# Kernel tuning notes

Measured on AMD Instinct MI355X. Metric: run time of the kernel, lower is better.

Reference implementation:

```python
import jax, jax.numpy as jnp
import numpy as np

B, L, C = 4, 2048, 1024

def setup_inputs() -> dict:
    key = jax.random.key(0)
    k1, k2, k3 = jax.random.split(key, 3)
    net_in = jax.random.normal(k1, (B, L, C), dtype=jnp.float32)
    # torch Linear weights stored as (out, in); we keep that convention
    w_qkv = jax.random.normal(k2, (3 * C, C), dtype=jnp.float32) * (1.0 / np.sqrt(C))
    w_out = jax.random.normal(k3, (C, C), dtype=jnp.float32) * (1.0 / np.sqrt(C))
    return {"net_in": net_in, "w_qkv": w_qkv, "w_out": w_out}

def reference(net_in, w_qkv, w_out):
    Bc, Lc, Cc = net_in.shape
    qkv = jnp.einsum('blc,dc->bld', net_in, w_qkv)  # (B, L, 3C)
    q, k, v = jnp.split(qkv, 3, axis=-1)
    attn = jnp.einsum('bqc,bkc->bqk', q, k) / jnp.sqrt(jnp.float32(Cc))
    causal = jnp.tril(jnp.ones((Lc, Lc), dtype=bool))
    attn = jnp.where(causal[None, :, :], attn, -jnp.inf)
    attn = jax.nn.softmax(attn, axis=-1)
    out = jnp.einsum('bqk,bkc->bqc', attn, v)
    return jnp.einsum('blc,dc->bld', out, w_out)
```

## Files before the change

### kernel.cpp

```cpp
#include <hip/hip_runtime.h>
#include <hip/hip_bf16.h>
#include <cstdint>
#include <cstddef>

typedef __hip_bfloat16 bf16;
typedef float  floatx4 __attribute__((ext_vector_type(4)));
typedef __bf16 bf16x8  __attribute__((ext_vector_type(8)));

typedef __attribute__((address_space(1))) void as1_void;
typedef __attribute__((address_space(3))) void as3_void;

constexpr int Bn = 4, Ln = 2048, Cn = 1024;

__device__ __forceinline__ void store_one(float* p, float v) { *p = v; }
__device__ __forceinline__ void store_one(bf16*  p, float v) { *p = __float2bfloat16(v); }

#define BAR()    asm volatile("s_barrier" ::: "memory")
#define VMCNT2() asm volatile("s_waitcnt vmcnt(2)" ::: "memory")
#define VMCNT0() asm volatile("s_waitcnt vmcnt(0)" ::: "memory")
#define SCHEDB() __builtin_amdgcn_sched_barrier(0)
#define STAGE(gp, off) \
    __builtin_amdgcn_global_load_lds((const as1_void*)(gp), (as3_void*)(smem + (off)), 16, 0, 0)

__device__ __forceinline__ void gemm256_core(
    char* __restrict__ smem,
    const bf16* __restrict__ A, const bf16* __restrict__ B,
    int m0, int n0, int kbeg, int kend, int lda, int ldb,
    floatx4 (&acc)[8][4])
{
    const int tid  = threadIdx.x;
    const int lane = tid & 63;
    const int quad = lane >> 4;
    const int lr   = lane & 15;
    const int wave = tid >> 6;
    const int wm   = (wave >> 2) * 128;
    const int wn   = (wave & 3) * 64;

#pragma unroll
    for (int i = 0; i < 8; ++i)
#pragma unroll
        for (int j = 0; j < 4; ++j) { floatx4 z = {0.f, 0.f, 0.f, 0.f}; acc[i][j] = z; }

    const int srow = tid >> 3;
    const int sx   = (tid & 7) ^ (srow & 7);
    const bf16* gA = A + (size_t)(m0 + srow) * lda + sx * 8 + kbeg;
    const bf16* gB = B + (size_t)(n0 + srow) * ldb + sx * 8 + kbeg;
    const int wuni = __builtin_amdgcn_readfirstlane((tid & 0x1C0) * 16);

    const int aoff = (wm + lr) * 64;
    const int boff = (wn + lr) * 64;
    const int s0   = (quad ^ (lr & 7)) * 8;

    const int NT = (kend - kbeg) >> 6;

    STAGE(gB,             32768 + 0 * 8192 + wuni);
    STAGE(gB + 64  * ldb, 32768 + 1 * 8192 + wuni);
    STAGE(gB + 128 * ldb, 32768 + 2 * 8192 + wuni);
    STAGE(gB + 192 * ldb, 32768 + 3 * 8192 + wuni);
    STAGE(gA,                     0 * 8192 + wuni);
    STAGE(gA + 128 * lda,         2 * 8192 + wuni);
    STAGE(gA + 64  * lda,         1 * 8192 + wuni);
    STAGE(gA + 192 * lda,         3 * 8192 + wuni);
    VMCNT2();
    BAR();

#define LDA4(MB, SK) do { _Pragma("unroll") for (int ii = 0; ii < 4; ++ii) \
        a[ii] = *(const bf16x8*)(As + aoff + ((MB) * 4 + ii) * 1024 + (SK)); } while (0)
#define LDB4(SK) do { _Pragma("unroll") for (int nn = 0; nn < 4; ++nn) \
        b[nn] = *(const bf16x8*)(Bs + boff + nn * 1024 + (SK)); } while (0)
#define MFMA16(MB) do { _Pragma("unroll") for (int ii = 0; ii < 4; ++ii) { \
        _Pragma("unroll") for (int nn = 0; nn < 4; ++nn) \
            acc[(MB) * 4 + ii][nn] = __builtin_amdgcn_mfma_f32_16x16x32_bf16( \
                a[ii], b[nn], acc[(MB) * 4 + ii][nn], 0, 0, 0); } } while (0)

    for (int t = 0; t < NT; ++t) {
        const bf16* As = (const bf16*)(smem + (t & 1) * 65536);
        const bf16* Bs = (const bf16*)(smem + (t & 1) * 65536 + 32768);
        const int  wl  = ((t + 1) & 1) * 65536;
        const int  kn  = (t + 1) << 6;
        const bool more = (t + 1 < NT);
        bf16x8 a[4], b[4];

        LDB4(s0);
        LDA4(0, s0);
        if (more) {
            STAGE(gB + kn,            wl + 32768 + 0 * 8192 + wuni);
            STAGE(gB + kn + 64 * ldb, wl + 32768 + 1 * 8192 + wuni);
        }
        BAR(); SCHEDB();
        __builtin_amdgcn_s_setprio(1);
        MFMA16(0);
        __builtin_amdgcn_s_setprio(0);
        SCHEDB();
        if (more) VMCNT2(); else VMCNT0();
        BAR();

        LDA4(1, s0);
        if (more) {
            STAGE(gB + kn + 128 * ldb, wl + 32768 + 2 * 8192 + wuni);
            STAGE(gB + kn + 192 * ldb, wl + 32768 + 3 * 8192 + wuni);
        }
        BAR(); SCHEDB();
        __builtin_amdgcn_s_setprio(1);
        MFMA16(1);
        __builtin_amdgcn_s_setprio(0);
        SCHEDB();
        BAR();

        LDB4(s0 ^ 32);
        LDA4(0, s0 ^ 32);
        if (more) {
            STAGE(gA + kn,             wl + 0 * 8192 + wuni);
            STAGE(gA + kn + 128 * lda, wl + 2 * 8192 + wuni);
        }
        BAR(); SCHEDB();
        __builtin_amdgcn_s_setprio(1);
        MFMA16(0);
        __builtin_amdgcn_s_setprio(0);
        SCHEDB();
        BAR();

        LDA4(1, s0 ^ 32);
        if (more) {
            STAGE(gA + kn + 64  * lda, wl + 1 * 8192 + wuni);
            STAGE(gA + kn + 192 * lda, wl + 3 * 8192 + wuni);
        }
        BAR(); SCHEDB();
        __builtin_amdgcn_s_setprio(1);
        MFMA16(1);
        __builtin_amdgcn_s_setprio(0);
        SCHEDB();
        if (more) VMCNT2();
        BAR();
    }
#undef LDA4
#undef LDB4
#undef MFMA16
}

template <typename OutT>
__device__ __forceinline__ void gemm256(
    char* __restrict__ smem,
    const bf16* __restrict__ A, const bf16* __restrict__ B, OutT* __restrict__ C,
    int m0, int n0, int kbeg, int kend, int lda, int ldb, int ldc, float cscale)
{
    floatx4 acc[8][4];
    gemm256_core(smem, A, B, m0, n0, kbeg, kend, lda, ldb, acc);

    const int lane = threadIdx.x & 63;
    const int quad = lane >> 4;
    const int lr   = lane & 15;
    const int wave = threadIdx.x >> 6;
    const int wm   = (wave >> 2) * 128;
    const int wn   = (wave & 3) * 64;

#pragma unroll
    for (int mi = 0; mi < 8; ++mi) {
        const int row = m0 + wm + mi * 16 + quad * 4;
#pragma unroll
        for (int n = 0; n < 4; ++n) {
            const int col = n0 + wn + n * 16 + lr;
            OutT* cp = C + (size_t)row * ldc + col;
#pragma unroll
            for (int r = 0; r < 4; ++r)
                store_one(cp + (size_t)r * ldc, acc[mi][n][r] * cscale);
        }
    }
}

__global__ __launch_bounds__(512, 2)
void g1_qk(const bf16* __restrict__ Xb, const bf16* __restrict__ Wqkb,
           bf16* __restrict__ QK)
{
    __shared__ __align__(16) char smem[131072];
    const int i = blockIdx.x;
    const int j = i >> 3;
    const int mt = (i & 7) * 4 + (j & 3);
    const int nt = j >> 2;
    gemm256<bf16>(smem, Xb, Wqkb, QK, mt * 256, nt * 256, 0, 1024, 1024, 1024, 2048, 1.0f);
}

__global__ __launch_bounds__(512, 2)
void g2_s_w2(const bf16* __restrict__ QK, const bf16* __restrict__ Wob,
             const bf16* __restrict__ WvT, bf16* __restrict__ S,
             bf16* __restrict__ W2)
{
    __shared__ __align__(16) char smem[131072];
    const int i = blockIdx.x;
    if (i < 144) {
        const int b = (i & 7) >> 1;
        const int t = (i >> 3) * 2 + (i & 1);
        int ti = (int)((sqrtf(8.f * t + 1.f) - 1.f) * 0.5f);
        while ((ti + 1) * (ti + 2) / 2 <= t) ++ti;
        while (ti * (ti + 1) / 2 > t) --ti;
        const int tj = t - ti * (ti + 1) / 2;
        const bf16* Aq = QK + (size_t)b * Ln * 2048;
        const bf16* Bk = Aq + 1024;
        bf16* Sb = S + (size_t)b * Ln * Ln;
        gemm256<bf16>(smem, Aq, Bk, Sb, ti * 256, tj * 256, 0, 1024, 2048, 2048, Ln, 0.03125f);
    } else {
        const int j = i - 144;
        gemm256<bf16>(smem, Wob, WvT, W2, (j & 3) * 256, (j >> 2) * 256, 0, 1024, 1024, 1024, 1024, 1.0f);
    }
}

__device__ __forceinline__ float waveMax(float x) {
#pragma unroll
    for (int o = 32; o > 0; o >>= 1) x = fmaxf(x, __shfl_xor(x, o, 64));
    return x;
}
__device__ __forceinline__ float waveSum(float x) {
#pragma unroll
    for (int o = 32; o > 0; o >>= 1) x += __shfl_xor(x, o, 64);
    return x;
}

__device__ void softmax_rows(bf16* __restrict__ S, int row0)
{
    const int wave = threadIdx.x >> 6, lane = threadIdx.x & 63;
    for (int it8 = 0; it8 < 8; ++it8) {
        const int row = row0 + wave * 8 + it8;
        const int q = row & (Ln - 1);
        bf16* Srow = S + (size_t)row * Ln;
        const int kmax = ((q >> 7) + 1) << 7;
        const int nv = (kmax + 511) >> 9;
        float x[4][8];
        float m = -1e30f;
        for (int it = 0; it < nv; ++it) {
            int c0 = it * 512 + lane * 8;
            bf16x8 v = *(const bf16x8*)(Srow + c0);
#pragma unroll
            for (int e = 0; e < 8; ++e) {
                float f = (float)v[e];
                f = (c0 + e <= q) ? f : -1e30f;
                x[it][e] = f;
                m = fmaxf(m, f);
            }
        }
        m = waveMax(m);
        float s = 0.f;
        for (int it = 0; it < nv; ++it)
#pragma unroll
            for (int e = 0; e < 8; ++e) {
                float ex = (x[it][e] > -1e29f) ? __expf(x[it][e] - m) : 0.f;
                x[it][e] = ex;
                s += ex;
            }
        s = waveSum(s);
        const float inv = 1.f / s;
        for (int it = 0; it < nv; ++it) {
            bf16x8 o;
#pragma unroll
            for (int e = 0; e < 8; ++e) o[e] = (__bf16)(x[it][e] * inv);
            *(bf16x8*)(Srow + it * 512 + lane * 8) = o;
        }
    }
}

__global__ __launch_bounds__(512, 2)
void g3_vwt_sm(const bf16* __restrict__ W2, const bf16* __restrict__ Xb,
               bf16* __restrict__ VWT, bf16* __restrict__ S)
{
    __shared__ __align__(16) char smem[131072];
    const int i = blockIdx.x;
    if (i < 128) {
        const int j = i >> 3;
        const int nt = (i & 7) * 4 + (j & 3);
        const int mt = j >> 2;
        gemm256<bf16>(smem, W2, Xb, VWT, mt * 256, nt * 256, 0, 1024, 1024, 1024, 8192, 1.0f);
    } else {
        softmax_rows(S, (i - 128) * 64);
    }
}

__global__ __launch_bounds__(512, 2)
void g4_out(const bf16* __restrict__ P, const bf16* __restrict__ VWT,
            float* __restrict__ out)
{
    __shared__ __align__(16) char smem[131072];
    const int i = blockIdx.x;
    const int r = i & 7;
    const int b = r >> 1, p = r & 1;
    const int q = i >> 3;
    const int nt = p * 2 + (q & 1);
    const int j = q >> 1;

    const bf16* Pp = P + (size_t)b * Ln * Ln;
    const bf16* Bv = VWT + (size_t)b * Ln;
    float* Co = out + (size_t)b * Ln * Cn;
    const int n0 = nt * 256;

    if (j < 4) {
        gemm256<float>(smem, Pp, Bv, Co, j * 256, n0, 0, (j + 1) * 256, Ln, 8192, Cn, 1.0f);
        return;
    }

    const int mt   = 4 + ((j - 4) >> 1);
    const int c    = (j - 4) & 1;
    const int half = ((mt + 1) * 256) >> 1;
    const int kb   = c * half;
    const int m0   = mt * 256;

    floatx4 acc[8][4];
    gemm256_core(smem, Pp, Bv, m0, n0, kb, kb + half, Ln, 8192, acc);

    const int lane = threadIdx.x & 63;
    const int quad = lane >> 4;
    const int lr   = lane & 15;
    const int wave = threadIdx.x >> 6;
    const int wm   = (wave >> 2) * 128;
    const int wn   = (wave & 3) * 64;

#pragma unroll
    for (int mi = 0; mi < 8; ++mi) {
        const int row = m0 + wm + mi * 16 + quad * 4;
#pragma unroll
        for (int n = 0; n < 4; ++n) {
            const int col = n0 + wn + n * 16 + lr;
            float* cp = Co + (size_t)row * Cn + col;
#pragma unroll
            for (int rr = 0; rr < 4; ++rr)
                unsafeAtomicAdd(cp + (size_t)rr * Cn, acc[mi][n][rr]);
        }
    }
}

__global__ __launch_bounds__(256)
void cast_all(const float* __restrict__ X, const float* __restrict__ Wqkv,
              const float* __restrict__ Wo,
              bf16* __restrict__ Xb, bf16* __restrict__ Wqkb,
              bf16* __restrict__ Wob, bf16* __restrict__ WvT,
              float* __restrict__ out)
{
    int blk = blockIdx.x;
    if (blk < 11264) {
        int i = blk * 256 + threadIdx.x;
        const float* src; bf16* dst; int off;
        if (i < 2097152)                 { src = X;    dst = Xb;   off = i; }
        else if (i < 2097152 + 524288)   { src = Wqkv; dst = Wqkb; off = i - 2097152; }
        else                             { src = Wo;   dst = Wob;  off = i - 2621440; }
        float4 f = ((const float4*)src)[off];
        bf16 o0 = __float2bfloat16(f.x), o1 = __float2bfloat16(f.y);
        bf16 o2 = __float2bfloat16(f.z), o3 = __float2bfloat16(f.w);
        ushort4 u;
        u.x = *(unsigned short*)&o0; u.y = *(unsigned short*)&o1;
        u.z = *(unsigned short*)&o2; u.w = *(unsigned short*)&o3;
        *(ushort4*)(dst + (size_t)off * 4) = u;
    } else if (blk < 12288) {
        __shared__ float t[32][33];
        int tt = blk - 11264;
        int c0 = (tt & 31) * 32;
        int r0 = (tt >> 5) * 32;
        const float* Wv = Wqkv + 2048 * 1024;
        int xcol = threadIdx.x & 31, y0 = threadIdx.x >> 5;
#pragma unroll
        for (int p = 0; p < 4; ++p) {
            int y = y0 + 8 * p;
            t[y][xcol] = Wv[(size_t)(r0 + y) * 1024 + c0 + xcol];
        }
        __syncthreads();
#pragma unroll
        for (int p = 0; p < 4; ++p) {
            int mloc = y0 + 8 * p;
            WvT[(size_t)(c0 + mloc) * 1024 + r0 + xcol] = __float2bfloat16(t[xcol][mloc]);
        }
    } else {
        int t = (blk - 12288) * 256 + threadIdx.x;
        float4* o4 = (float4*)out;
        float4 z = {0.f, 0.f, 0.f, 0.f};
#pragma unroll
        for (int p = 0; p < 4; ++p)
            o4[(size_t)p * 524288 + 262144 + t] = z;
    }
}

extern "C" void kernel_launch(void* const* d_in, const int* in_sizes, int n_in,
                              void* d_out, int out_size, void* d_ws, size_t ws_size,
                              hipStream_t stream)
{
    const float* X    = (const float*)d_in[0];
    const float* Wqkv = (const float*)d_in[1];
    const float* Wout = (const float*)d_in[2];
    float* out = (float*)d_out;

    char* ws = (char*)d_ws;
    const size_t MiB = 1024ull * 1024ull;
    bf16* Xb   = (bf16*)(ws + 0);
    bf16* QK   = (bf16*)(ws + 16 * MiB);
    bf16* VWT  = (bf16*)(ws + 48 * MiB);
    bf16* Sbuf = (bf16*)(ws + 64 * MiB);
    bf16* Wqkb = (bf16*)(ws + 96 * MiB);
    bf16* WvT  = (bf16*)(ws + 100 * MiB);
    bf16* Wob  = (bf16*)(ws + 102 * MiB);
    bf16* W2   = (bf16*)(ws + 104 * MiB);

    cast_all<<<dim3(13312), 256, 0, stream>>>(X, Wqkv, Wout, Xb, Wqkb, Wob, WvT, out);

    g1_qk<<<dim3(256), 512, 0, stream>>>(Xb, Wqkb, QK);

    g2_s_w2<<<dim3(160), 512, 0, stream>>>(QK, Wob, WvT, Sbuf, W2);

    g3_vwt_sm<<<dim3(256), 512, 0, stream>>>(W2, Xb, VWT, Sbuf);

    g4_out<<<dim3(192), 512, 0, stream>>>(Sbuf, VWT, out);
}
```

Before: 239.4 us.

## Replace split-K atomic PV GEMM with 256x128 tiles and direct stores

The final P·VWT GEMM now uses a new 256x128-tile kernel over 256 blocks, each covering the full causal K range for its row tile. This replaces 256x256 tiles where the later row tiles were split in K and summed with float atomics. Because every output is now written exactly once, the zero-fill of the output in the cast kernel is removed. The trade-off is more total A-tile loads (each P row tile is read by twice as many column tiles) and uneven work across blocks, since late row tiles run long K loops without splitting. LDS use drops to 96KB.

```diff
diff --git a/kernel.cpp b/kernel.cpp
--- a/kernel.cpp
+++ b/kernel.cpp
@@ -164,6 +164,130 @@
 #pragma unroll
             for (int r = 0; r < 4; ++r)
                 store_one(cp + (size_t)r * ldc, acc[mi][n][r] * cscale);
+        }
+    }
+}
+
+__device__ __forceinline__ void gemm_pv_128n(
+    char* __restrict__ smem,
+    const bf16* __restrict__ A, const bf16* __restrict__ B, float* __restrict__ C,
+    int m0, int n0, int kend, int lda, int ldb, int ldc)
+{
+    const int tid  = threadIdx.x;
+    const int lane = tid & 63;
+    const int quad = lane >> 4;
+    const int lr   = lane & 15;
+    const int wave = tid >> 6;
+    const int wm   = (wave >> 2) * 128;
+    const int wn   = (wave & 3) * 32;
+
+    floatx4 acc[8][2];
+#pragma unroll
+    for (int i = 0; i < 8; ++i)
+#pragma unroll
+        for (int j = 0; j < 2; ++j) { floatx4 z = {0.f, 0.f, 0.f, 0.f}; acc[i][j] = z; }
+
+    const int srow = tid >> 3;
+    const int sx   = (tid & 7) ^ (srow & 7);
+    const bf16* gA = A + (size_t)(m0 + srow) * lda + sx * 8;
+    const bf16* gB = B + (size_t)(n0 + srow) * ldb + sx * 8;
+    const int wuni = __builtin_amdgcn_readfirstlane((tid & 0x1C0) * 16);
+
+    const int aoff = (wm + lr) * 64;
+    const int boff = (wn + lr) * 64;
+    const int s0   = (quad ^ (lr & 7)) * 8;
+
+    const int NT = kend >> 6;
+    const int BUF = 49152;
+
+    STAGE(gB,             32768 + 0 * 8192 + wuni);
+    STAGE(gB + 64  * ldb, 32768 + 1 * 8192 + wuni);
+    STAGE(gA,                     0 * 8192 + wuni);
+    STAGE(gA + 128 * lda,         2 * 8192 + wuni);
+    STAGE(gA + 64  * lda,         1 * 8192 + wuni);
+    STAGE(gA + 192 * lda,         3 * 8192 + wuni);
+    VMCNT2();
+    BAR();
+
+#define LDA4(MB, SK) do { _Pragma("unroll") for (int ii = 0; ii < 4; ++ii) \
+        a[ii] = *(const bf16x8*)(As + aoff + ((MB) * 4 + ii) * 1024 + (SK)); } while (0)
+#define LDB2(SK) do { _Pragma("unroll") for (int nn = 0; nn < 2; ++nn) \
+        b[nn] = *(const bf16x8*)(Bs + boff + nn * 1024 + (SK)); } while (0)
+#define MFMA8(MB) do { _Pragma("unroll") for (int ii = 0; ii < 4; ++ii) { \
+        _Pragma("unroll") for (int nn = 0; nn < 2; ++nn) \
+            acc[(MB) * 4 + ii][nn] = __builtin_amdgcn_mfma_f32_16x16x32_bf16( \
+                a[ii], b[nn], acc[(MB) * 4 + ii][nn], 0, 0, 0); } } while (0)
+
+    for (int t = 0; t < NT; ++t) {
+        const bf16* As = (const bf16*)(smem + (t & 1) * BUF);
+        const bf16* Bs = (const bf16*)(smem + (t & 1) * BUF + 32768);
+        const int  wl  = ((t + 1) & 1) * BUF;
+        const int  kn  = (t + 1) << 6;
+        const bool more = (t + 1 < NT);
+        bf16x8 a[4], b[2];
+
+        LDB2(s0);
+        LDA4(0, s0);
+        if (more) {
+            STAGE(gB + kn,            wl + 32768 + 0 * 8192 + wuni);
+            STAGE(gB + kn + 64 * ldb, wl + 32768 + 1 * 8192 + wuni);
+        }
+        BAR(); SCHEDB();
+        __builtin_amdgcn_s_setprio(1);
+        MFMA8(0);
+        __builtin_amdgcn_s_setprio(0);
+        SCHEDB();
+        if (more) VMCNT2(); else VMCNT0();
+        BAR();
+
+        LDA4(1, s0);
+        if (more) {
+            STAGE(gA + kn,             wl + 0 * 8192 + wuni);
+            STAGE(gA + kn + 128 * lda, wl + 2 * 8192 + wuni);
+        }
+        BAR(); SCHEDB();
+        __builtin_amdgcn_s_setprio(1);
+        MFMA8(1);
+        __builtin_amdgcn_s_setprio(0);
+        SCHEDB();
+        BAR();
+
+        LDB2(s0 ^ 32);
+        LDA4(0, s0 ^ 32);
+        if (more) {
+            STAGE(gA + kn + 64  * lda, wl + 1 * 8192 + wuni);
+            STAGE(gA + kn + 192 * lda, wl + 3 * 8192 + wuni);
+        }
+        BAR(); SCHEDB();
+        __builtin_amdgcn_s_setprio(1);
+        MFMA8(0);
+        __builtin_amdgcn_s_setprio(0);
+        SCHEDB();
+        BAR();
+
+        LDA4(1, s0 ^ 32);
+        BAR(); SCHEDB();
+        __builtin_amdgcn_s_setprio(1);
+        MFMA8(1);
+        __builtin_amdgcn_s_setprio(0);
+        SCHEDB();
+        if (more) VMCNT2();
+        BAR();
+    }
+#undef LDA4
+#undef LDB2
+#undef MFMA8
+
+#pragma unroll
+    for (int mi = 0; mi < 8; ++mi) {
+        const int row = m0 + wm + mi * 16 + quad * 4;
+#pragma unroll
+        for (int n = 0; n < 2; ++n) {
+            const int col = n0 + wn + n * 16 + lr;
+            float* cp = C + (size_t)row * ldc + col;
+#pragma unroll
+            for (int r = 0; r < 4; ++r)
+                cp[(size_t)r * ldc] = acc[mi][n][r];
         }
     }
 }
@@ -277,60 +401,25 @@
 void g4_out(const bf16* __restrict__ P, const bf16* __restrict__ VWT,
             float* __restrict__ out)
 {
-    __shared__ __align__(16) char smem[131072];
+    __shared__ __align__(16) char smem[98304];
     const int i = blockIdx.x;
     const int r = i & 7;
     const int b = r >> 1, p = r & 1;
     const int q = i >> 3;
-    const int nt = p * 2 + (q & 1);
-    const int j = q >> 1;
+    const int nt = p * 4 + (q & 3);
+    const int mt = q >> 2;
 
     const bf16* Pp = P + (size_t)b * Ln * Ln;
     const bf16* Bv = VWT + (size_t)b * Ln;
     float* Co = out + (size_t)b * Ln * Cn;
-    const int n0 = nt * 256;
-
-    if (j < 4) {
-        gemm256<float>(smem, Pp, Bv, Co, j * 256, n0, 0, (j + 1) * 256, Ln, 8192, Cn, 1.0f);
-        return;
-    }
-
-    const int mt   = 4 + ((j - 4) >> 1);
-    const int c    = (j - 4) & 1;
-    const int half = ((mt + 1) * 256) >> 1;
-    const int kb   = c * half;
-    const int m0   = mt * 256;
-
-    floatx4 acc[8][4];
-    gemm256_core(smem, Pp, Bv, m0, n0, kb, kb + half, Ln, 8192, acc);
-
-    const int lane = threadIdx.x & 63;
-    const int quad = lane >> 4;
-    const int lr   = lane & 15;
-    const int wave = threadIdx.x >> 6;
-    const int wm   = (wave >> 2) * 128;
-    const int wn   = (wave & 3) * 64;
-
-#pragma unroll
-    for (int mi = 0; mi < 8; ++mi) {
-        const int row = m0 + wm + mi * 16 + quad * 4;
-#pragma unroll
-        for (int n = 0; n < 4; ++n) {
-            const int col = n0 + wn + n * 16 + lr;
-            float* cp = Co + (size_t)row * Cn + col;
-#pragma unroll
-            for (int rr = 0; rr < 4; ++rr)
-                unsafeAtomicAdd(cp + (size_t)rr * Cn, acc[mi][n][rr]);
-        }
-    }
+    gemm_pv_128n(smem, Pp, Bv, Co, mt * 256, nt * 128, (mt + 1) * 256, Ln, 8192, Cn);
 }
 
 __global__ __launch_bounds__(256)
 void cast_all(const float* __restrict__ X, const float* __restrict__ Wqkv,
               const float* __restrict__ Wo,
               bf16* __restrict__ Xb, bf16* __restrict__ Wqkb,
-              bf16* __restrict__ Wob, bf16* __restrict__ WvT,
-              float* __restrict__ out)
+              bf16* __restrict__ Wob, bf16* __restrict__ WvT)
 {
     int blk = blockIdx.x;
     if (blk < 11264) {
@@ -346,7 +435,7 @@
         u.x = *(unsigned short*)&o0; u.y = *(unsigned short*)&o1;
         u.z = *(unsigned short*)&o2; u.w = *(unsigned short*)&o3;
         *(ushort4*)(dst + (size_t)off * 4) = u;
-    } else if (blk < 12288) {
+    } else {
         __shared__ float t[32][33];
         int tt = blk - 11264;
         int c0 = (tt & 31) * 32;
@@ -364,13 +453,6 @@
             int mloc = y0 + 8 * p;
             WvT[(size_t)(c0 + mloc) * 1024 + r0 + xcol] = __float2bfloat16(t[xcol][mloc]);
         }
-    } else {
-        int t = (blk - 12288) * 256 + threadIdx.x;
-        float4* o4 = (float4*)out;
-        float4 z = {0.f, 0.f, 0.f, 0.f};
-#pragma unroll
-        for (int p = 0; p < 4; ++p)
-            o4[(size_t)p * 524288 + 262144 + t] = z;
     }
 }
 
@@ -394,7 +476,7 @@
     bf16* Wob  = (bf16*)(ws + 102 * MiB);
     bf16* W2   = (bf16*)(ws + 104 * MiB);
 
-    cast_all<<<dim3(13312), 256, 0, stream>>>(X, Wqkv, Wout, Xb, Wqkb, Wob, WvT, out);
+    cast_all<<<dim3(12288), 256, 0, stream>>>(X, Wqkv, Wout, Xb, Wqkb, Wob, WvT);
 
     g1_qk<<<dim3(256), 512, 0, stream>>>(Xb, Wqkb, QK);
 
@@ -402,5 +484,5 @@
 
     g3_vwt_sm<<<dim3(256), 512, 0, stream>>>(W2, Xb, VWT, Sbuf);
 
-    g4_out<<<dim3(192), 512, 0, stream>>>(Sbuf, VWT, out);
-}
+    g4_out<<<dim3(256), 512, 0, stream>>>(Sbuf, VWT, out);
+}
```

New measurement: 224.0 us. -6.4%, faster.
